# Optimization experiments

Measured on AMD Instinct MI355X. Metric: run time of the kernel, lower is better.

Reference implementation:

```python
import jax, jax.numpy as jnp
import numpy as np
import math

B, S, E, H = 2, 4096, 1024, 1024

def setup_inputs() -> dict:
    key = jax.random.key(0)
    ks = jax.random.split(key, 7)
    X = jax.random.normal(ks[0], (B, S, E), dtype=jnp.float32)
    attention_mask = jnp.ones((B, S, S), dtype=jnp.int32)
    sc = 1.0 / math.sqrt(E)
    Wq = jax.random.normal(ks[1], (H, E), dtype=jnp.float32) * sc
    Wk = jax.random.normal(ks[2], (H, E), dtype=jnp.float32) * sc
    Wv = jax.random.normal(ks[3], (H, E), dtype=jnp.float32) * sc
    bq = jnp.zeros((H,), dtype=jnp.float32)
    bk = jnp.zeros((H,), dtype=jnp.float32)
    bv = jnp.zeros((H,), dtype=jnp.float32)
    return {"X": X, "attention_mask": attention_mask,
            "Wq": Wq, "bq": bq, "Wk": Wk, "bk": bk, "Wv": Wv, "bv": bv}

def reference(X, attention_mask, Wq, bq, Wk, bk, Wv, bv):
    # Linear layers: y = x @ W^T + b (torch convention W is [out, in])
    Q = jnp.einsum('bse,he->bsh', X, Wq) + bq
    K = jnp.einsum('bse,he->bsh', X, Wk) + bk
    V = jnp.einsum('bse,he->bsh', X, Wv) + bv
    scale = 1.0 / math.sqrt(H)
    scores = jnp.einsum('bqh,bkh->bqk', Q, K) * scale  # [B,S,S]
    scores = jnp.where(attention_mask == 0, -jnp.inf, scores)
    # dropout (eval mode -> identity) would be applied here, BEFORE softmax
    weights = jax.nn.softmax(scores, axis=-1)
    out = jnp.einsum('bqk,bkh->bqh', weights, V)  # [B,S,H]
    return out
```

## Files before the change

kernel.cpp:

```cpp
#include <hip/hip_runtime.h>
#include <stdint.h>


typedef __bf16 bf16;
typedef __attribute__((ext_vector_type(4))) __bf16 bf16x4;
typedef __attribute__((ext_vector_type(8))) __bf16 bf16x8;
typedef __attribute__((ext_vector_type(4))) float f32x4;
typedef __attribute__((ext_vector_type(4))) int i32x4;

__device__ __forceinline__ void g2l16(const void* g, void* l) {
  __builtin_amdgcn_global_load_lds(
      (const __attribute__((address_space(1))) uint32_t*)g,
      (__attribute__((address_space(3))) uint32_t*)l, 16, 0, 0);
}

__global__ __launch_bounds__(256) void prep(
    const float* __restrict__ X, const float* __restrict__ Wq,
    const float* __restrict__ Wk, const float* __restrict__ Wv,
    const int* __restrict__ mask, bf16* __restrict__ X_bf,
    bf16* __restrict__ W_bf, uint32_t* __restrict__ mbits)
{
  const int b = blockIdx.x;
  if (b < 4096) {
    const int i = (b * 256 + threadIdx.x) * 8;
    f32x4 a = *(const f32x4*)(X + i);
    f32x4 c = *(const f32x4*)(X + i + 4);
    bf16x8 o;
#pragma unroll
    for (int e = 0; e < 4; ++e) { o[e] = (bf16)a[e]; o[4 + e] = (bf16)c[e]; }
    *(bf16x8*)(X_bf + i) = o;
  } else if (b < 5632) {
    const int i = ((b - 4096) * 256 + threadIdx.x) * 8;
    const int seg = i >> 20;
    const int off = i & 1048575;
    const float* src = (seg == 0) ? Wq : (seg == 1) ? Wk : Wv;
    f32x4 a = *(const f32x4*)(src + off);
    f32x4 c = *(const f32x4*)(src + off + 4);
    bf16x8 o;
#pragma unroll
    for (int e = 0; e < 4; ++e) { o[e] = (bf16)a[e]; o[4 + e] = (bf16)c[e]; }
    *(bf16x8*)(W_bf + i) = o;
  } else {
    const int t = (b - 5632) * 256 + threadIdx.x;
    const int* p = mask + (size_t)t * 32;
    uint32_t w = 0;
#pragma unroll
    for (int ch = 0; ch < 8; ++ch) {
      i32x4 v = *(const i32x4*)(p + ch * 4);
#pragma unroll
      for (int e = 0; e < 4; ++e)
        if (v[e] != 0) w |= 1u << (ch * 4 + e);
    }
    mbits[t] = w;
  }
}


__global__ __launch_bounds__(256, 2) void gemm_qkv(
    const bf16* __restrict__ Xb, const bf16* __restrict__ Wb3,
    const float* __restrict__ bq, const float* __restrict__ bk,
    const float* __restrict__ bv, bf16* __restrict__ QK,
    bf16* __restrict__ Vt)
{
  constexpr int K = 1024, N = 1024;
  __shared__ __align__(16) bf16 ldsA[128 * 64];
  __shared__ __align__(16) bf16 ldsB[128 * 64];

  const int tid  = threadIdx.x;
  const int lane = tid & 63;
  const int wave = tid >> 6;
  const int which = blockIdx.y >> 3;
  const int n0 = (blockIdx.y & 7) * 128;
  const int m0 = blockIdx.x * 128;
  const bf16* Bt = Wb3 + (size_t)which * 1048576;
  const float* bias = (which == 0) ? bq : ((which == 1) ? bk : bv);

  const int l15  = lane & 15;
  const int quad = lane >> 4;
  const int wm = (wave >> 1) * 64;
  const int wn = (wave & 1) * 64;
  const int sw = l15 & 7;

  f32x4 acc[4][4];
#pragma unroll
  for (int i = 0; i < 4; ++i)
#pragma unroll
    for (int j = 0; j < 4; ++j) acc[i][j] = f32x4{0.f, 0.f, 0.f, 0.f};

  const int srow = tid >> 3;
  const int scol = ((tid & 7) ^ (srow & 7)) * 8;
  const size_t a_base = (size_t)(m0 + srow) * K + scol;
  const size_t b_base = (size_t)(n0 + srow) * K + scol;
  const int lds_off = tid * 8;

  for (int kt = 0; kt < K; kt += 64) {
    const bf16* ga = Xb + a_base + kt;
    const bf16* gb = Bt + b_base + kt;
#pragma unroll
    for (int it = 0; it < 4; ++it) {
      g2l16(ga + (size_t)(it * 32) * K, &ldsA[lds_off + it * 2048]);
      g2l16(gb + (size_t)(it * 32) * K, &ldsB[lds_off + it * 2048]);
    }
    __syncthreads();
#pragma unroll
    for (int ks = 0; ks < 2; ++ks) {
      const int ch = ks * 4 + quad;
      bf16x8 af[4], bfg[4];
#pragma unroll
      for (int i = 0; i < 4; ++i)
        af[i] = *(const bf16x8*)&ldsA[(wm + i * 16 + l15) * 64 + (ch ^ sw) * 8];
#pragma unroll
      for (int j = 0; j < 4; ++j)
        bfg[j] = *(const bf16x8*)&ldsB[(wn + j * 16 + l15) * 64 + (ch ^ sw) * 8];
#pragma unroll
      for (int i = 0; i < 4; ++i)
#pragma unroll
        for (int j = 0; j < 4; ++j)
          acc[i][j] = __builtin_amdgcn_mfma_f32_16x16x32_bf16(
              af[i], bfg[j], acc[i][j], 0, 0, 0);
    }
    __syncthreads();
  }

  if (which < 2) {
    bf16* C = QK + (size_t)which * (size_t)(8192 * 1024);
#pragma unroll
    for (int i = 0; i < 4; ++i) {
#pragma unroll
      for (int j = 0; j < 4; ++j) {
        const int r = m0 + wm + i * 16 + quad * 4;
        const int c = n0 + wn + j * 16 + l15;
        const float bvv = bias[c];
        f32x4 v = acc[i][j];
#pragma unroll
        for (int reg = 0; reg < 4; ++reg)
          C[(size_t)(r + reg) * N + c] = (bf16)(v[reg] + bvv);
      }
    }
  } else {
#pragma unroll
    for (int i = 0; i < 4; ++i) {
#pragma unroll
      for (int j = 0; j < 4; ++j) {
        const int r = m0 + wm + i * 16 + quad * 4;
        const int c = n0 + wn + j * 16 + l15;
        const int b = r >> 12, s = r & 4095;
        const float bvv = bias[c];
        f32x4 v = acc[i][j];
        bf16x4 o;
#pragma unroll
        for (int reg = 0; reg < 4; ++reg) o[reg] = (bf16)(v[reg] + bvv);
        *(bf16x4*)&Vt[((size_t)(b * 1024 + c)) * 4096 + s] = o;
      }
    }
  }
}

__global__ __launch_bounds__(256, 2) void gemm_scores(
    const bf16* __restrict__ A, const bf16* __restrict__ Bt,
    const uint64_t* __restrict__ mb, bf16* __restrict__ P,
    float* __restrict__ row_sum)
{
  constexpr int N = 4096, K = 1024;
  __shared__ __align__(16) bf16 ldsA[128 * 64];
  __shared__ __align__(16) bf16 ldsB[128 * 64];

  const int tid  = threadIdx.x;
  const int lane = tid & 63;
  const int wave = tid >> 6;
  const int m0 = blockIdx.x * 128;
  const int n0 = blockIdx.y * 128;
  const int batch = m0 >> 12;
  const bf16* Btb = Bt + (size_t)batch * (size_t)(4096 * 1024);

  const int l15  = lane & 15;
  const int quad = lane >> 4;
  const int wm = (wave >> 1) * 64;
  const int wn = (wave & 1) * 64;
  const int sw = l15 & 7;

  f32x4 acc[4][4];
#pragma unroll
  for (int i = 0; i < 4; ++i)
#pragma unroll
    for (int j = 0; j < 4; ++j) acc[i][j] = f32x4{0.f, 0.f, 0.f, 0.f};

  const int srow = tid >> 3;
  const int scol = ((tid & 7) ^ (srow & 7)) * 8;
  const size_t a_base = (size_t)(m0 + srow) * K + scol;
  const size_t b_base = (size_t)(n0 + srow) * K + scol;
  const int lds_off = tid * 8;

  for (int kt = 0; kt < K; kt += 64) {
    const bf16* ga = A + a_base + kt;
    const bf16* gb = Btb + b_base + kt;
#pragma unroll
    for (int it = 0; it < 4; ++it) {
      g2l16(ga + (size_t)(it * 32) * K, &ldsA[lds_off + it * 2048]);
      g2l16(gb + (size_t)(it * 32) * K, &ldsB[lds_off + it * 2048]);
    }
    __syncthreads();
#pragma unroll
    for (int ks = 0; ks < 2; ++ks) {
      const int ch = ks * 4 + quad;
      bf16x8 af[4], bfg[4];
#pragma unroll
      for (int i = 0; i < 4; ++i)
        af[i] = *(const bf16x8*)&ldsA[(wm + i * 16 + l15) * 64 + (ch ^ sw) * 8];
#pragma unroll
      for (int j = 0; j < 4; ++j)
        bfg[j] = *(const bf16x8*)&ldsB[(wn + j * 16 + l15) * 64 + (ch ^ sw) * 8];
#pragma unroll
      for (int i = 0; i < 4; ++i)
#pragma unroll
        for (int j = 0; j < 4; ++j)
          acc[i][j] = __builtin_amdgcn_mfma_f32_16x16x32_bf16(
              af[i], bfg[j], acc[i][j], 0, 0, 0);
    }
    __syncthreads();
  }

#pragma unroll
  for (int i = 0; i < 4; ++i) {
    const int rb = m0 + wm + i * 16 + quad * 4;
    uint64_t w[4];
#pragma unroll
    for (int reg = 0; reg < 4; ++reg)
      w[reg] = mb[((size_t)(rb + reg) * N + (n0 + wn)) >> 6];
    f32x4 rsum = f32x4{0.f, 0.f, 0.f, 0.f};
#pragma unroll
    for (int j = 0; j < 4; ++j) {
      const int c = n0 + wn + j * 16 + l15;
      f32x4 v = acc[i][j];
#pragma unroll
      for (int reg = 0; reg < 4; ++reg) {
        float e = __expf(v[reg] * 0.03125f);
        if (!((w[reg] >> (j * 16 + l15)) & 1)) e = 0.f;
        P[(size_t)(rb + reg) * N + c] = (bf16)e;
        rsum[reg] += e;
      }
    }
#pragma unroll
    for (int off = 1; off < 16; off <<= 1) {
#pragma unroll
      for (int reg = 0; reg < 4; ++reg)
        rsum[reg] += __shfl_xor(rsum[reg], off);
    }
    if (l15 == 0) {
#pragma unroll
      for (int reg = 0; reg < 4; ++reg)
        atomicAdd(&row_sum[rb + reg], rsum[reg]);
    }
  }
}

__global__ __launch_bounds__(256, 2) void gemm_pv(
    const bf16* __restrict__ A, const bf16* __restrict__ Bt,
    const float* __restrict__ row_sum, float* __restrict__ C)
{
  constexpr int N = 1024, K = 4096;
  __shared__ __align__(16) bf16 ldsA[128 * 64];
  __shared__ __align__(16) bf16 ldsB[128 * 64];

  const int tid  = threadIdx.x;
  const int lane = tid & 63;
  const int wave = tid >> 6;
  const int m0 = blockIdx.x * 128;
  const int n0 = blockIdx.y * 128;
  const int batch = m0 >> 12;
  const bf16* Btb = Bt + (size_t)batch * (size_t)(1024 * 4096);

  const int l15  = lane & 15;
  const int quad = lane >> 4;
  const int wm = (wave >> 1) * 64;
  const int wn = (wave & 1) * 64;
  const int sw = l15 & 7;

  f32x4 acc[4][4];
#pragma unroll
  for (int i = 0; i < 4; ++i)
#pragma unroll
    for (int j = 0; j < 4; ++j) acc[i][j] = f32x4{0.f, 0.f, 0.f, 0.f};

  const int srow = tid >> 3;
  const int scol = ((tid & 7) ^ (srow & 7)) * 8;
  const size_t a_base = (size_t)(m0 + srow) * K + scol;
  const size_t b_base = (size_t)(n0 + srow) * K + scol;
  const int lds_off = tid * 8;

  for (int kt = 0; kt < K; kt += 64) {
    const bf16* ga = A + a_base + kt;
    const bf16* gb = Btb + b_base + kt;
#pragma unroll
    for (int it = 0; it < 4; ++it) {
      g2l16(ga + (size_t)(it * 32) * K, &ldsA[lds_off + it * 2048]);
      g2l16(gb + (size_t)(it * 32) * K, &ldsB[lds_off + it * 2048]);
    }
    __syncthreads();
#pragma unroll
    for (int ks = 0; ks < 2; ++ks) {
      const int ch = ks * 4 + quad;
      bf16x8 af[4], bfg[4];
#pragma unroll
      for (int i = 0; i < 4; ++i)
        af[i] = *(const bf16x8*)&ldsA[(wm + i * 16 + l15) * 64 + (ch ^ sw) * 8];
#pragma unroll
      for (int j = 0; j < 4; ++j)
        bfg[j] = *(const bf16x8*)&ldsB[(wn + j * 16 + l15) * 64 + (ch ^ sw) * 8];
#pragma unroll
      for (int i = 0; i < 4; ++i)
#pragma unroll
        for (int j = 0; j < 4; ++j)
          acc[i][j] = __builtin_amdgcn_mfma_f32_16x16x32_bf16(
              af[i], bfg[j], acc[i][j], 0, 0, 0);
    }
    __syncthreads();
  }

#pragma unroll
  for (int i = 0; i < 4; ++i) {
    const int r = m0 + wm + i * 16 + quad * 4;
    f32x4 inv;
#pragma unroll
    for (int reg = 0; reg < 4; ++reg) inv[reg] = 1.0f / row_sum[r + reg];
#pragma unroll
    for (int j = 0; j < 4; ++j) {
      const int c = n0 + wn + j * 16 + l15;
      f32x4 v = acc[i][j];
#pragma unroll
      for (int reg = 0; reg < 4; ++reg)
        C[(size_t)(r + reg) * N + c] = v[reg] * inv[reg];
    }
  }
}

extern "C" void kernel_launch(void* const* d_in, const int* in_sizes, int n_in,
                              void* d_out, int out_size, void* d_ws,
                              size_t ws_size, hipStream_t stream) {
  const float* X   = (const float*)d_in[0];
  const int* mask  = (const int*)d_in[1];
  const float* Wq  = (const float*)d_in[2];
  const float* bq  = (const float*)d_in[3];
  const float* Wk  = (const float*)d_in[4];
  const float* bk  = (const float*)d_in[5];
  const float* Wv  = (const float*)d_in[6];
  const float* bv  = (const float*)d_in[7];
  float* out = (float*)d_out;

  const size_t QKV_ELEMS = (size_t)8192 * 1024;
  bf16* Q    = (bf16*)d_ws;
  bf16* Kb   = Q + QKV_ELEMS;
  bf16* X_bf = Kb + QKV_ELEMS;
  bf16* Vt   = X_bf + QKV_ELEMS;
  bf16* Sc   = Vt + QKV_ELEMS;
  bf16* W_bf = Sc;
  float* row_sum = (float*)X_bf;
  uint32_t* mbits = (uint32_t*)d_out;

  const dim3 blk(256);
  prep<<<dim3(9728), blk, 0, stream>>>(X, Wq, Wk, Wv, mask, X_bf, W_bf, mbits);
  gemm_qkv<<<dim3(64, 24), blk, 0, stream>>>(X_bf, W_bf, bq, bk, bv, Q, Vt);
  hipMemsetAsync(row_sum, 0, 8192 * sizeof(float), stream);
  gemm_scores<<<dim3(64, 32), blk, 0, stream>>>(
      Q, Kb, (const uint64_t*)mbits, Sc, row_sum);
  gemm_pv<<<dim3(64, 8), blk, 0, stream>>>(Sc, Vt, row_sum, out);
}
```

Baseline: 446.5 us.

## Fold mask bit-packing into QKV GEMM launch as extra ballot-based blocks

```diff
diff --git a/kernel.cpp b/kernel.cpp
--- a/kernel.cpp
+++ b/kernel.cpp
@@ -6,7 +6,6 @@
 typedef __attribute__((ext_vector_type(4))) __bf16 bf16x4;
 typedef __attribute__((ext_vector_type(8))) __bf16 bf16x8;
 typedef __attribute__((ext_vector_type(4))) float f32x4;
-typedef __attribute__((ext_vector_type(4))) int i32x4;
 
 __device__ __forceinline__ void g2l16(const void* g, void* l) {
   __builtin_amdgcn_global_load_lds(
@@ -17,42 +16,30 @@
 __global__ __launch_bounds__(256) void prep(
     const float* __restrict__ X, const float* __restrict__ Wq,
     const float* __restrict__ Wk, const float* __restrict__ Wv,
-    const int* __restrict__ mask, bf16* __restrict__ X_bf,
-    bf16* __restrict__ W_bf, uint32_t* __restrict__ mbits)
+    bf16* __restrict__ X_bf, bf16* __restrict__ W_bf)
 {
   const int b = blockIdx.x;
+  const float* src;
+  bf16* dst;
+  int i;
   if (b < 4096) {
-    const int i = (b * 256 + threadIdx.x) * 8;
-    f32x4 a = *(const f32x4*)(X + i);
-    f32x4 c = *(const f32x4*)(X + i + 4);
-    bf16x8 o;
-#pragma unroll
-    for (int e = 0; e < 4; ++e) { o[e] = (bf16)a[e]; o[4 + e] = (bf16)c[e]; }
-    *(bf16x8*)(X_bf + i) = o;
-  } else if (b < 5632) {
-    const int i = ((b - 4096) * 256 + threadIdx.x) * 8;
+    i = (b * 256 + threadIdx.x) * 8;
+    src = X; dst = X_bf;
+  } else {
+    i = ((b - 4096) * 256 + threadIdx.x) * 8;
     const int seg = i >> 20;
-    const int off = i & 1048575;
-    const float* src = (seg == 0) ? Wq : (seg == 1) ? Wk : Wv;
-    f32x4 a = *(const f32x4*)(src + off);
-    f32x4 c = *(const f32x4*)(src + off + 4);
-    bf16x8 o;
-#pragma unroll
-    for (int e = 0; e < 4; ++e) { o[e] = (bf16)a[e]; o[4 + e] = (bf16)c[e]; }
-    *(bf16x8*)(W_bf + i) = o;
-  } else {
-    const int t = (b - 5632) * 256 + threadIdx.x;
-    const int* p = mask + (size_t)t * 32;
-    uint32_t w = 0;
-#pragma unroll
-    for (int ch = 0; ch < 8; ++ch) {
-      i32x4 v = *(const i32x4*)(p + ch * 4);
-#pragma unroll
-      for (int e = 0; e < 4; ++e)
-        if (v[e] != 0) w |= 1u << (ch * 4 + e);
-    }
-    mbits[t] = w;
-  }
+    src = (seg == 0) ? Wq : (seg == 1) ? Wk : Wv;
+    dst = W_bf + (i & ~1048575);
+    i &= 1048575;
+    dst += i - i;
+    dst = W_bf + (seg << 20);
+  }
+  f32x4 a = *(const f32x4*)(src + i);
+  f32x4 c = *(const f32x4*)(src + i + 4);
+  bf16x8 o;
+#pragma unroll
+  for (int e = 0; e < 4; ++e) { o[e] = (bf16)a[e]; o[4 + e] = (bf16)c[e]; }
+  *(bf16x8*)(dst + i) = o;
 }
 
 
@@ -60,15 +47,30 @@
     const bf16* __restrict__ Xb, const bf16* __restrict__ Wb3,
     const float* __restrict__ bq, const float* __restrict__ bk,
     const float* __restrict__ bv, bf16* __restrict__ QK,
-    bf16* __restrict__ Vt)
+    bf16* __restrict__ Vt, const int* __restrict__ mask,
+    uint64_t* __restrict__ mbits)
 {
   constexpr int K = 1024, N = 1024;
-  __shared__ __align__(16) bf16 ldsA[128 * 64];
-  __shared__ __align__(16) bf16 ldsB[128 * 64];
-
   const int tid  = threadIdx.x;
   const int lane = tid & 63;
   const int wave = tid >> 6;
+
+  if (blockIdx.y >= 24) {
+    const int mb_block = (blockIdx.y - 24) * 64 + blockIdx.x;
+    const int w0 = mb_block * 2048 + wave * 512;
+#pragma unroll 4
+    for (int it = 0; it < 512; ++it) {
+      const int w = w0 + it;
+      const int v = mask[(size_t)w * 64 + lane];
+      const uint64_t bal = __ballot(v != 0);
+      if (lane == 0) mbits[w] = bal;
+    }
+    return;
+  }
+
+  __shared__ __align__(16) bf16 ldsA[128 * 64];
+  __shared__ __align__(16) bf16 ldsB[128 * 64];
+
   const int which = blockIdx.y >> 3;
   const int n0 = (blockIdx.y & 7) * 128;
   const int m0 = blockIdx.x * 128;
@@ -355,13 +357,13 @@
   bf16* Sc   = Vt + QKV_ELEMS;
   bf16* W_bf = Sc;
   float* row_sum = (float*)X_bf;
-  uint32_t* mbits = (uint32_t*)d_out;
+  uint64_t* mbits = (uint64_t*)d_out;
 
   const dim3 blk(256);
-  prep<<<dim3(9728), blk, 0, stream>>>(X, Wq, Wk, Wv, mask, X_bf, W_bf, mbits);
-  gemm_qkv<<<dim3(64, 24), blk, 0, stream>>>(X_bf, W_bf, bq, bk, bv, Q, Vt);
+  prep<<<dim3(5632), blk, 0, stream>>>(X, Wq, Wk, Wv, X_bf, W_bf);
+  gemm_qkv<<<dim3(64, 28), blk, 0, stream>>>(X_bf, W_bf, bq, bk, bv, Q, Vt,
+                                             mask, mbits);
   hipMemsetAsync(row_sum, 0, 8192 * sizeof(float), stream);
-  gemm_scores<<<dim3(64, 32), blk, 0, stream>>>(
-      Q, Kb, (const uint64_t*)mbits, Sc, row_sum);
+  gemm_scores<<<dim3(64, 32), blk, 0, stream>>>(Q, Kb, mbits, Sc, row_sum);
   gemm_pv<<<dim3(64, 8), blk, 0, stream>>>(Sc, Vt, row_sum, out);
 }
```

Result: slower. 631.8 us (+41.5%).
